# Optimization experiments

Measured on AMD Instinct MI355X. Metric: run time of the kernel, lower is better.

Reference implementation:

```python
import jax, jax.numpy as jnp
import numpy as np


def setup_inputs() -> dict:
    key = jax.random.key(0)
    ks = jax.random.split(key, 5)
    B, S, C, H = 32, 512, 320, 512
    scale = 1.0 / np.sqrt(H)
    return {
        "x": jax.random.normal(ks[0], (B, S, C), dtype=jnp.float32),
        "w_ih": jax.random.normal(ks[1], (4 * H, S), dtype=jnp.float32) * scale,
        "w_hh": jax.random.normal(ks[2], (4 * H, H), dtype=jnp.float32) * scale,
        "b_ih": jax.random.normal(ks[3], (4 * H,), dtype=jnp.float32) * scale,
        "b_hh": jax.random.normal(ks[4], (4 * H,), dtype=jnp.float32) * scale,
    }


def reference(x, w_ih, w_hh, b_ih, b_hh):
    # x: (B, S, C). Original permutes to (B, C, S) and runs a length-1 LSTM per
    # channel with zero initial state -> single LSTM cell step:
    #   gates = x_c @ W_ih^T + b_ih + b_hh   (W_hh @ h0 == 0)
    # PyTorch gate order: i, f, g, o.
    B, S, C = x.shape
    H = w_hh.shape[1]
    gates = jnp.einsum("bsc,gs->bcg", x, w_ih) + b_ih + b_hh  # (B, C, 4H)
    i_g, f_g, g_g, o_g = jnp.split(gates, 4, axis=-1)
    c = jax.nn.sigmoid(i_g) * jnp.tanh(g_g)           # c0 = 0
    h = jax.nn.sigmoid(o_g) * jnp.tanh(c)             # (B, C, H)
    # Faithful to torch: cat over channels along batch dim -> (C*B, H),
    # then reshape to (B, C, H) (scrambles batch/channel order).
    h = jnp.transpose(h, (1, 0, 2)).reshape(B, C, H)
    # dropout is identity in eval mode
    return jnp.transpose(h, (0, 2, 1))                # (B, H, C)
```

## Files before the change

kernel.cpp:

```cpp
#include <hip/hip_runtime.h>
#include <stdint.h>

#define B_  32
#define S_  512
#define C_  320
#define H_  512
#define NROW (B_*C_)

typedef __attribute__((ext_vector_type(8))) short short8;
typedef __attribute__((ext_vector_type(4))) float f32x4;

__device__ __forceinline__ unsigned short f2bf(float x){
  unsigned u = __builtin_bit_cast(unsigned, x);
  u = u + 0x7FFFu + ((u >> 16) & 1u);
  return (unsigned short)(u >> 16);
}
__device__ __forceinline__ float bf2f(unsigned short h){
  unsigned u = ((unsigned)h) << 16;
  return __builtin_bit_cast(float, u);
}
__device__ __forceinline__ float sigf(float x){ return 1.0f/(1.0f + __expf(-x)); }
__device__ __forceinline__ float tanh_fast(float x){ return 2.0f/(1.0f + __expf(-2.0f*x)) - 1.0f; }

__device__ __forceinline__ void gload16(const void* g, void* l){
  __builtin_amdgcn_global_load_lds((const __attribute__((address_space(1))) void*)g,
                                   (__attribute__((address_space(3))) void*)l, 16, 0, 0);
}

__global__ __launch_bounds__(256) void k_cast_w(const float* __restrict__ w,
                                                unsigned short* __restrict__ aws){
  int flat = blockIdx.x*256 + threadIdx.x;
  int plane = flat >> 16;
  int rem   = flat & 65535;
  int srow  = (plane == 0 ? 0 : (plane == 1 ? 1024 : 1536));
  float4 v = ((const float4*)w)[srow*128 + rem];
  uint2 p;
  p.x = (unsigned)f2bf(v.x) | ((unsigned)f2bf(v.y) << 16);
  p.y = (unsigned)f2bf(v.z) | ((unsigned)f2bf(v.w) << 16);
  ((uint2*)aws)[flat] = p;
}

__global__ __launch_bounds__(256) void k_cast_tx(const float* __restrict__ x,
                                                 unsigned short* __restrict__ xws){
  __shared__ float lds[64][65];
  const int tid = threadIdx.x;
  const int st = blockIdx.x, ctt = blockIdx.y, b = blockIdx.z;
  const int s0 = st*64, c0 = ctt*64;
  const int row = tid >> 2, q = tid & 3;

  const float* src = x + ((size_t)(b*S_ + s0 + row))*C_ + c0 + q*16;
  #pragma unroll
  for (int j = 0; j < 4; j++){
    float4 v = ((const float4*)src)[j];
    lds[row][q*16 + j*4 + 0] = v.x;
    lds[row][q*16 + j*4 + 1] = v.y;
    lds[row][q*16 + j*4 + 2] = v.z;
    lds[row][q*16 + j*4 + 3] = v.w;
  }
  __syncthreads();
  const int crow = row;
  #pragma unroll
  for (int j = 0; j < 2; j++){
    short8 o;
    #pragma unroll
    for (int e = 0; e < 8; e++)
      o[e] = (short)f2bf(lds[q*16 + j*8 + e][crow]);
    *(short8*)(xws + ((size_t)(b*C_ + c0 + crow))*S_ + s0 + q*16 + j*8) = o;
  }
}

__global__ __launch_bounds__(512, 2) void k_gemm(const unsigned short* __restrict__ aws,
                                                 const unsigned short* __restrict__ xws,
                                                 const float* __restrict__ b_ih,
                                                 const float* __restrict__ b_hh,
                                                 unsigned short* __restrict__ hws){
  __shared__ alignas(16) char lds[2][65536];

  const int tid  = threadIdx.x;
  const int w    = tid >> 6;
  const int lane = tid & 63;
  const int wm = w >> 2, wn = w & 3;

  const int flat = blockIdx.x;
  const int xcd = flat & 7, j = flat >> 3;
  const int b  = ((j >> 3) << 3) + xcd;
  const int kt = j & 7;
  const int k0 = kt*64;

  f32x4 acc[3][2][5];
  #pragma unroll
  for (int gi = 0; gi < 3; gi++)
    #pragma unroll
    for (int mf = 0; mf < 2; mf++)
      #pragma unroll
      for (int nf = 0; nf < 5; nf++)
        acc[gi][mf][nf] = (f32x4){0.f, 0.f, 0.f, 0.f};

  const int cr   = lane >> 3;
  const int slot = ((lane & 7) ^ cr) << 4;

  const char* srcp[8];
  char*       dstp[8];
  #pragma unroll
  for (int i = 0; i < 8; i++){
    int q = w*8 + i;
    if (q < 24){
      int gi = q >> 3, q8 = q & 7;
      int grow = gi*512 + k0 + q8*8 + cr;
      srcp[i] = (const char*)aws + ((size_t)grow*S_)*2 + slot;
      dstp[i] = &lds[0][0] + gi*8192 + q8*1024;
    } else {
      int q8 = q - 24;
      int xrow = b*C_ + q8*8 + cr;
      srcp[i] = (const char*)xws + ((size_t)xrow*S_)*2 + slot;
      dstp[i] = &lds[0][0] + 24576 + q8*1024;
    }
  }

  #pragma unroll
  for (int i = 0; i < 8; i++){ gload16(srcp[i], dstp[i]); srcp[i] += 128; }
  __syncthreads();

  const int lo16 = (lane >> 4) << 4;
  const int swz  = (lane & 7) << 4;
  const int l15  = lane & 15;

  for (int t = 0; t < 8; t++){
    const int p = t & 1;
    if (t < 7){
      #pragma unroll
      for (int i = 0; i < 8; i++){
        gload16(srcp[i], dstp[i] + ((p^1) << 16));
        srcp[i] += 128;
      }
    }
    const char* base = &lds[p][0];
    #pragma unroll
    for (int ks = 0; ks < 2; ks++){
      const int colb = (ks*64 + lo16) ^ swz;
      short8 aF[3][2], bF[5];
      #pragma unroll
      for (int gi = 0; gi < 3; gi++)
        #pragma unroll
        for (int mf = 0; mf < 2; mf++)
          aF[gi][mf] = *(const short8*)(base + gi*8192 + (wm*32 + mf*16 + l15)*128 + colb);
      #pragma unroll
      for (int nf = 0; nf < 5; nf++)
        bF[nf] = *(const short8*)(base + 24576 + (wn*80 + nf*16 + l15)*128 + colb);
      #pragma unroll
      for (int gi = 0; gi < 3; gi++)
        #pragma unroll
        for (int mf = 0; mf < 2; mf++)
          #pragma unroll
          for (int nf = 0; nf < 5; nf++)
            acc[gi][mf][nf] = __builtin_amdgcn_mfma_f32_16x16x32_bf16(aF[gi][mf], bF[nf], acc[gi][mf][nf], 0, 0, 0);
    }
    __syncthreads();
  }

  #pragma unroll
  for (int mf = 0; mf < 2; mf++){
    const int kb = k0 + wm*32 + mf*16 + ((lane >> 4) << 2);
    float bi[4], bg[4], bo[4];
    #pragma unroll
    for (int r = 0; r < 4; r++){
      bi[r] = b_ih[kb + r]        + b_hh[kb + r];
      bg[r] = b_ih[1024 + kb + r] + b_hh[1024 + kb + r];
      bo[r] = b_ih[1536 + kb + r] + b_hh[1536 + kb + r];
    }
    #pragma unroll
    for (int nf = 0; nf < 5; nf++){
      const int c = wn*80 + nf*16 + l15;
      const size_t n = (size_t)c*32 + (size_t)b;
      float h[4];
      #pragma unroll
      for (int r = 0; r < 4; r++){
        float iv = acc[0][mf][nf][r] + bi[r];
        float gv = acc[1][mf][nf][r] + bg[r];
        float ov = acc[2][mf][nf][r] + bo[r];
        float cc = sigf(iv) * tanh_fast(gv);
        h[r] = sigf(ov) * tanh_fast(cc);
      }
      uint2 p2;
      p2.x = (unsigned)f2bf(h[0]) | ((unsigned)f2bf(h[1]) << 16);
      p2.y = (unsigned)f2bf(h[2]) | ((unsigned)f2bf(h[3]) << 16);
      *(uint2*)(hws + n*H_ + kb) = p2;
    }
  }
}

__global__ __launch_bounds__(256) void k_out(const unsigned short* __restrict__ hws,
                                             float* __restrict__ out){
  __shared__ float lds[64][65];
  const int tid = threadIdx.x;
  const int kt = blockIdx.x, ctt = blockIdx.y, b2 = blockIdx.z;
  const int k0 = kt*64, n0 = b2*320 + ctt*64;
  const int rr = tid >> 2, q = tid & 3;

  #pragma unroll
  for (int j = 0; j < 2; j++){
    short8 v = *(const short8*)(hws + ((size_t)(n0 + rr))*H_ + k0 + q*16 + j*8);
    #pragma unroll
    for (int e = 0; e < 8; e++)
      lds[rr][q*16 + j*8 + e] = bf2f((unsigned short)v[e]);
  }
  __syncthreads();
  const int krow = rr;
  #pragma unroll
  for (int j = 0; j < 4; j++){
    int c2l = q*16 + j*4;
    float4 o;
    o.x = lds[c2l + 0][krow];
    o.y = lds[c2l + 1][krow];
    o.z = lds[c2l + 2][krow];
    o.w = lds[c2l + 3][krow];
    *(float4*)(out + (size_t)b2*(H_*C_) + (size_t)(k0 + krow)*C_ + ctt*64 + c2l) = o;
  }
}

extern "C" void kernel_launch(void* const* d_in, const int* in_sizes, int n_in,
                              void* d_out, int out_size, void* d_ws, size_t ws_size,
                              hipStream_t stream){
  const float* x    = (const float*)d_in[0];
  const float* w_ih = (const float*)d_in[1];
  const float* b_ih = (const float*)d_in[3];
  const float* b_hh = (const float*)d_in[4];
  float* out = (float*)d_out;

  char* ws = (char*)d_ws;
  unsigned short* aws = (unsigned short*)(ws);
  unsigned short* xws = (unsigned short*)(ws + 2097152);
  unsigned short* hws = (unsigned short*)(ws + 2097152 + 10485760);

  k_cast_w <<<768, 256, 0, stream>>>(w_ih, aws);
  k_cast_tx<<<dim3(8, 5, 32), 256, 0, stream>>>(x, xws);
  k_gemm   <<<256, 512, 0, stream>>>(aws, xws, b_ih, b_hh, hws);
  k_out    <<<dim3(8, 5, 32), 256, 0, stream>>>(hws, out);
}
```

Measured before the change: 52.56 us.

## Retile GEMM to 128-column N tiles with single-buffered LDS and more blocks

The GEMM now flattens batch and channel into one N dimension and tiles it in chunks of 128 instead of one batch's 320 channels. It launches 640 blocks of 256 threads instead of 256 blocks of 512, with 3 blocks per CU. The LDS double buffer is replaced by one 40KB buffer with load-then-sync per K step, so occupancy and tail balance go up. In exchange the copy/compute overlap is lost and the epilogue needs an integer divide per output column.

```diff
diff --git a/kernel.cpp b/kernel.cpp
--- a/kernel.cpp
+++ b/kernel.cpp
@@ -69,90 +69,85 @@
   }
 }
 
-__global__ __launch_bounds__(512, 2) void k_gemm(const unsigned short* __restrict__ aws,
+__global__ __launch_bounds__(256, 3) void k_gemm(const unsigned short* __restrict__ aws,
                                                  const unsigned short* __restrict__ xws,
                                                  const float* __restrict__ b_ih,
                                                  const float* __restrict__ b_hh,
                                                  unsigned short* __restrict__ hws){
-  __shared__ alignas(16) char lds[2][65536];
+  __shared__ alignas(16) char lds[40960];
 
   const int tid  = threadIdx.x;
   const int w    = tid >> 6;
   const int lane = tid & 63;
-  const int wm = w >> 2, wn = w & 3;
-
-  const int flat = blockIdx.x;
-  const int xcd = flat & 7, j = flat >> 3;
-  const int b  = ((j >> 3) << 3) + xcd;
-  const int kt = j & 7;
+  const int wm = w >> 1, wn = w & 1;
+
+  const int bid = blockIdx.x;
+  const int x8 = bid & 7, y = bid >> 3;
+  const int kt = y & 7, n2 = y >> 3;
+  const int nt = n2*8 + x8;
   const int k0 = kt*64;
-
-  f32x4 acc[3][2][5];
+  const int nbase = nt*128;
+
+  f32x4 acc[3][2][4];
   #pragma unroll
   for (int gi = 0; gi < 3; gi++)
     #pragma unroll
     for (int mf = 0; mf < 2; mf++)
       #pragma unroll
-      for (int nf = 0; nf < 5; nf++)
+      for (int nf = 0; nf < 4; nf++)
         acc[gi][mf][nf] = (f32x4){0.f, 0.f, 0.f, 0.f};
 
   const int cr   = lane >> 3;
   const int slot = ((lane & 7) ^ cr) << 4;
 
-  const char* srcp[8];
-  char*       dstp[8];
-  #pragma unroll
-  for (int i = 0; i < 8; i++){
-    int q = w*8 + i;
+  const char* wsb = (const char*)aws;
+  unsigned srcoff[10];
+  int      dstoff[10];
+  #pragma unroll
+  for (int i = 0; i < 10; i++){
+    int q = w*10 + i;
     if (q < 24){
       int gi = q >> 3, q8 = q & 7;
       int grow = gi*512 + k0 + q8*8 + cr;
-      srcp[i] = (const char*)aws + ((size_t)grow*S_)*2 + slot;
-      dstp[i] = &lds[0][0] + gi*8192 + q8*1024;
+      srcoff[i] = (unsigned)(grow*1024 + slot);
+      dstoff[i] = gi*8192 + q8*1024;
     } else {
       int q8 = q - 24;
-      int xrow = b*C_ + q8*8 + cr;
-      srcp[i] = (const char*)xws + ((size_t)xrow*S_)*2 + slot;
-      dstp[i] = &lds[0][0] + 24576 + q8*1024;
-    }
-  }
-
-  #pragma unroll
-  for (int i = 0; i < 8; i++){ gload16(srcp[i], dstp[i]); srcp[i] += 128; }
-  __syncthreads();
+      int xrow = nbase + q8*8 + cr;
+      srcoff[i] = (unsigned)(2097152 + xrow*1024 + slot);
+      dstoff[i] = 24576 + q8*1024;
+    }
+  }
 
   const int lo16 = (lane >> 4) << 4;
   const int swz  = (lane & 7) << 4;
   const int l15  = lane & 15;
 
   for (int t = 0; t < 8; t++){
-    const int p = t & 1;
-    if (t < 7){
-      #pragma unroll
-      for (int i = 0; i < 8; i++){
-        gload16(srcp[i], dstp[i] + ((p^1) << 16));
-        srcp[i] += 128;
-      }
-    }
-    const char* base = &lds[p][0];
+    #pragma unroll
+    for (int i = 0; i < 10; i++){
+      gload16(wsb + (size_t)srcoff[i], &lds[0] + dstoff[i]);
+      srcoff[i] += 128;
+    }
+    __syncthreads();
     #pragma unroll
     for (int ks = 0; ks < 2; ks++){
       const int colb = (ks*64 + lo16) ^ swz;
-      short8 aF[3][2], bF[5];
+      short8 aF[3][2], bF[4];
       #pragma unroll
       for (int gi = 0; gi < 3; gi++)
         #pragma unroll
         for (int mf = 0; mf < 2; mf++)
-          aF[gi][mf] = *(const short8*)(base + gi*8192 + (wm*32 + mf*16 + l15)*128 + colb);
-      #pragma unroll
-      for (int nf = 0; nf < 5; nf++)
-        bF[nf] = *(const short8*)(base + 24576 + (wn*80 + nf*16 + l15)*128 + colb);
+          aF[gi][mf] = *(const short8*)(&lds[0] + gi*8192 + (wm*32 + mf*16 + l15)*128 + colb);
+      #pragma unroll
+      for (int nf = 0; nf < 4; nf++)
+        bF[nf] = *(const short8*)(&lds[0] + 24576 + (wn*64 + nf*16 + l15)*128 + colb);
       #pragma unroll
       for (int gi = 0; gi < 3; gi++)
         #pragma unroll
         for (int mf = 0; mf < 2; mf++)
           #pragma unroll
-          for (int nf = 0; nf < 5; nf++)
+          for (int nf = 0; nf < 4; nf++)
             acc[gi][mf][nf] = __builtin_amdgcn_mfma_f32_16x16x32_bf16(aF[gi][mf], bF[nf], acc[gi][mf][nf], 0, 0, 0);
     }
     __syncthreads();
@@ -169,22 +164,24 @@
       bo[r] = b_ih[1536 + kb + r] + b_hh[1536 + kb + r];
     }
     #pragma unroll
-    for (int nf = 0; nf < 5; nf++){
-      const int c = wn*80 + nf*16 + l15;
-      const size_t n = (size_t)c*32 + (size_t)b;
+    for (int nf = 0; nf < 4; nf++){
+      const int n = nbase + wn*64 + nf*16 + l15;
+      const int bb = n / 320;
+      const int cc = n - bb*320;
+      const size_t nr = (size_t)cc*32 + (size_t)bb;
       float h[4];
       #pragma unroll
       for (int r = 0; r < 4; r++){
         float iv = acc[0][mf][nf][r] + bi[r];
         float gv = acc[1][mf][nf][r] + bg[r];
         float ov = acc[2][mf][nf][r] + bo[r];
-        float cc = sigf(iv) * tanh_fast(gv);
-        h[r] = sigf(ov) * tanh_fast(cc);
+        float ce = sigf(iv) * tanh_fast(gv);
+        h[r] = sigf(ov) * tanh_fast(ce);
       }
       uint2 p2;
       p2.x = (unsigned)f2bf(h[0]) | ((unsigned)f2bf(h[1]) << 16);
       p2.y = (unsigned)f2bf(h[2]) | ((unsigned)f2bf(h[3]) << 16);
-      *(uint2*)(hws + n*H_ + kb) = p2;
+      *(uint2*)(hws + nr*H_ + kb) = p2;
     }
   }
 }
@@ -234,6 +231,6 @@
 
   k_cast_w <<<768, 256, 0, stream>>>(w_ih, aws);
   k_cast_tx<<<dim3(8, 5, 32), 256, 0, stream>>>(x, xws);
-  k_gemm   <<<256, 512, 0, stream>>>(aws, xws, b_ih, b_hh, hws);
+  k_gemm   <<<640, 256, 0, stream>>>(aws, xws, b_ih, b_hh, hws);
   k_out    <<<dim3(8, 5, 32), 256, 0, stream>>>(hws, out);
 }
```

After: 55.58 us. 5.8% more time.

## Restructure GEMM main loop pipeline with two tiles in flight and explicit waitcnt

Applied to the files above, without the earlier changes.

The k_gemm loop now prefetches two K-tiles ahead. Each iteration loads all LDS fragments into registers, hits a barrier, issues the async global->LDS loads for tile t+2 into the buffer it just freed, then runs the MFMAs. Partial vmcnt waits replace full __syncthreads, and sched_barriers keep the compiler from reordering, so memory latency overlaps better with compute. The loop is fully unrolled and addressing uses 32-bit offsets from a single workspace base. The cost is higher register pressure from holding both k-steps of fragments, which could hurt occupancy under launch_bounds(512,2).

```diff
diff --git a/kernel.cpp b/kernel.cpp
--- a/kernel.cpp
+++ b/kernel.cpp
@@ -81,8 +81,8 @@
   const int lane = tid & 63;
   const int wm = w >> 2, wn = w & 3;
 
-  const int flat = blockIdx.x;
-  const int xcd = flat & 7, j = flat >> 3;
+  const int bid = blockIdx.x;
+  const int xcd = bid & 7, j = bid >> 3;
   const int b  = ((j >> 3) << 3) + xcd;
   const int kt = j & 7;
   const int k0 = kt*64;
@@ -99,63 +99,84 @@
   const int cr   = lane >> 3;
   const int slot = ((lane & 7) ^ cr) << 4;
 
-  const char* srcp[8];
-  char*       dstp[8];
+  const char* wsb = (const char*)aws;
+  unsigned srcoff[8];
+  int      dstoff[8];
   #pragma unroll
   for (int i = 0; i < 8; i++){
     int q = w*8 + i;
     if (q < 24){
       int gi = q >> 3, q8 = q & 7;
       int grow = gi*512 + k0 + q8*8 + cr;
-      srcp[i] = (const char*)aws + ((size_t)grow*S_)*2 + slot;
-      dstp[i] = &lds[0][0] + gi*8192 + q8*1024;
+      srcoff[i] = (unsigned)(grow*1024 + slot);
+      dstoff[i] = gi*8192 + q8*1024;
     } else {
       int q8 = q - 24;
       int xrow = b*C_ + q8*8 + cr;
-      srcp[i] = (const char*)xws + ((size_t)xrow*S_)*2 + slot;
-      dstp[i] = &lds[0][0] + 24576 + q8*1024;
-    }
-  }
-
-  #pragma unroll
-  for (int i = 0; i < 8; i++){ gload16(srcp[i], dstp[i]); srcp[i] += 128; }
-  __syncthreads();
+      srcoff[i] = (unsigned)(2097152 + xrow*1024 + slot);
+      dstoff[i] = 24576 + q8*1024;
+    }
+  }
+
+  #pragma unroll
+  for (int i = 0; i < 8; i++) gload16(wsb + (size_t)srcoff[i],       &lds[0][0] + dstoff[i]);
+  #pragma unroll
+  for (int i = 0; i < 8; i++) gload16(wsb + (size_t)(srcoff[i]+128), &lds[0][0] + dstoff[i] + 65536);
+  asm volatile("s_waitcnt vmcnt(8)" ::: "memory");
+  __builtin_amdgcn_sched_barrier(0);
+  __builtin_amdgcn_s_barrier();
 
   const int lo16 = (lane >> 4) << 4;
   const int swz  = (lane & 7) << 4;
   const int l15  = lane & 15;
-
+  const int arow0 = (wm*32 + l15)*128;
+  const int brow0 = (wn*80 + l15)*128;
+
+  #pragma unroll
   for (int t = 0; t < 8; t++){
     const int p = t & 1;
-    if (t < 7){
-      #pragma unroll
-      for (int i = 0; i < 8; i++){
-        gload16(srcp[i], dstp[i] + ((p^1) << 16));
-        srcp[i] += 128;
-      }
-    }
-    const char* base = &lds[p][0];
+    char* base = &lds[0][0] + (p << 16);
+
+    short8 aF[2][3][2], bF[2][5];
     #pragma unroll
     for (int ks = 0; ks < 2; ks++){
       const int colb = (ks*64 + lo16) ^ swz;
-      short8 aF[3][2], bF[5];
       #pragma unroll
       for (int gi = 0; gi < 3; gi++)
         #pragma unroll
         for (int mf = 0; mf < 2; mf++)
-          aF[gi][mf] = *(const short8*)(base + gi*8192 + (wm*32 + mf*16 + l15)*128 + colb);
+          aF[ks][gi][mf] = *(const short8*)(base + gi*8192 + arow0 + mf*2048 + colb);
       #pragma unroll
       for (int nf = 0; nf < 5; nf++)
-        bF[nf] = *(const short8*)(base + 24576 + (wn*80 + nf*16 + l15)*128 + colb);
+        bF[ks][nf] = *(const short8*)(base + 24576 + brow0 + nf*2048 + colb);
+    }
+    asm volatile("s_waitcnt lgkmcnt(0)" ::: "memory");
+    __builtin_amdgcn_sched_barrier(0);
+    __builtin_amdgcn_s_barrier();
+
+    if (t < 6){
+      #pragma unroll
+      for (int i = 0; i < 8; i++)
+        gload16(wsb + (size_t)(srcoff[i] + (unsigned)(t+2)*128), base + dstoff[i]);
+      __builtin_amdgcn_sched_barrier(0);
+    }
+
+    #pragma unroll
+    for (int ks = 0; ks < 2; ks++)
       #pragma unroll
       for (int gi = 0; gi < 3; gi++)
         #pragma unroll
         for (int mf = 0; mf < 2; mf++)
           #pragma unroll
           for (int nf = 0; nf < 5; nf++)
-            acc[gi][mf][nf] = __builtin_amdgcn_mfma_f32_16x16x32_bf16(aF[gi][mf], bF[nf], acc[gi][mf][nf], 0, 0, 0);
-    }
-    __syncthreads();
+            acc[gi][mf][nf] = __builtin_amdgcn_mfma_f32_16x16x32_bf16(aF[ks][gi][mf], bF[ks][nf], acc[gi][mf][nf], 0, 0, 0);
+
+    if (t < 7){
+      if (t < 6){ asm volatile("s_waitcnt vmcnt(8)" ::: "memory"); }
+      else      { asm volatile("s_waitcnt vmcnt(0)" ::: "memory"); }
+      __builtin_amdgcn_sched_barrier(0);
+      __builtin_amdgcn_s_barrier();
+    }
   }
 
   #pragma unroll
@@ -171,20 +192,20 @@
     #pragma unroll
     for (int nf = 0; nf < 5; nf++){
       const int c = wn*80 + nf*16 + l15;
-      const size_t n = (size_t)c*32 + (size_t)b;
+      const size_t nr = (size_t)c*32 + (size_t)b;
       float h[4];
       #pragma unroll
       for (int r = 0; r < 4; r++){
         float iv = acc[0][mf][nf][r] + bi[r];
         float gv = acc[1][mf][nf][r] + bg[r];
         float ov = acc[2][mf][nf][r] + bo[r];
-        float cc = sigf(iv) * tanh_fast(gv);
-        h[r] = sigf(ov) * tanh_fast(cc);
+        float ce = sigf(iv) * tanh_fast(gv);
+        h[r] = sigf(ov) * tanh_fast(ce);
       }
       uint2 p2;
       p2.x = (unsigned)f2bf(h[0]) | ((unsigned)f2bf(h[1]) << 16);
       p2.y = (unsigned)f2bf(h[2]) | ((unsigned)f2bf(h[3]) << 16);
-      *(uint2*)(hws + n*H_ + kb) = p2;
+      *(uint2*)(hws + nr*H_ + kb) = p2;
     }
   }
 }
```

After: 53.19 us. About the same (+1.2%).
